# Optimization experiments

Hardware: AMD Instinct MI355X
Metric: run time of the kernel (lower is better)

## Reference

```python
import jax, jax.numpy as jnp
from jax import lax
import numpy as np

P = 7            # patch_size
NP = 10          # n_patches
WIN = 20         # window_size
STRIDE = 4       # window loop stride
EMB = 128        # embedding_dimension
L = WIN - P + 1  # valid-conv output side (14)
HALF = WIN // 2 - P // 2  # window start offset before clipping (7)


def _positions(H, W):
    # x outer, y inner, exactly matching the nested python loops in the source
    return np.array([(x, y) for x in range(0, H - WIN + 1, STRIDE)
                     for y in range(0, W - WIN + 1, STRIDE)], dtype=np.int32)


def _forward(images, Wp, bp, pos_emb, Wb, bb):
    B, C, H, W = images.shape
    BC = B * C
    pos = jnp.asarray(_positions(H, W))  # [Ppos, 2]

    def per_pos(p):
        x, y = p[0], p[1]
        xb0 = jnp.maximum(x - HALF, 0)          # clipped window start (x / cols)
        yb0 = jnp.maximum(y - HALF, 0)          # clipped window start (y / rows)
        winW = jnp.minimum(x - HALF + WIN, W) - xb0  # clipped window width
        winH = jnp.minimum(y - HALF + WIN, H) - yb0  # clipped window height
        # reference patch: rows y:y+P, cols x:x+P (from ORIGINAL data, as in source)
        ref = lax.dynamic_slice(images, (0, 0, y, x), (B, C, P, P)).reshape(BC, 1, P, P)
        # fixed-size window slice; upper bound never clips for our dims, lower-clip
        # handled by masking invalid candidate offsets below
        win = lax.dynamic_slice(images, (0, 0, yb0, xb0), (B, C, WIN, WIN)).reshape(BC, WIN, WIN)
        # grouped cross-correlation == torch conv2d(groups=BC) similarity
        sim = lax.conv_general_dilated(win[None], ref, (1, 1), 'VALID',
                                       feature_group_count=BC,
                                       dimension_numbers=('NCHW', 'OIHW', 'NCHW'))[0]  # [BC,L,L]
        valid = (jnp.arange(L)[:, None] <= winH - P) & (jnp.arange(L)[None, :] <= winW - P)
        sim = jnp.where(valid[None], sim, -jnp.inf)
        _, idx = lax.top_k(sim.reshape(BC, L * L), NP)  # [BC, NP]
        oy, ox = idx // L, idx % L  # row / col offsets inside the window

        def extract(w2, a, b):
            # source's meshgrid indexing yields the TRANSPOSED patch, flattened
            return lax.dynamic_slice(w2, (a, b), (P, P)).T.reshape(P * P)
        patches = jax.vmap(jax.vmap(extract, in_axes=(None, 0, 0)))(win, oy, ox)  # [BC,NP,P*P]
        # source bug kept: x_coords = row offset + x window start (and vice versa)
        return patches, oy + xb0, ox + yb0

    patches, xi, yi = jax.vmap(per_pos)(pos)  # [Ppos,BC,NP,49], [Ppos,BC,NP] int32 x2

    # NOTE: the TransformerEncoder output is discarded in the source; the actual
    # math is back_projection(projection(patches) + pos_emb).
    emb = patches.reshape(-1, B, C, NP, P * P) @ Wp + bp + pos_emb  # [Ppos,B,C,NP,EMB]
    den = (emb @ Wb + bb).reshape(-1, BC, NP, P, P)                 # [Ppos,BC,NP,P,P]

    img0 = images.reshape(BC, H, W)
    cnt0 = jnp.ones((BC, H, W), images.dtype)

    def upd(im, cn, x_i, y_i, d):
        reg = lax.dynamic_slice(im, (y_i, x_i), (P, P))
        c = lax.dynamic_slice(cn, (y_i, x_i), (P, P))
        im = lax.dynamic_update_slice(im, (reg * c + d) / (c + 1.0), (y_i, x_i))
        # source bug kept: counter incremented at transposed slice [x, y]
        ct = lax.dynamic_slice(cn, (x_i, y_i), (P, P)) + 1.0
        cn = lax.dynamic_update_slice(cn, ct, (x_i, y_i))
        return im, cn
    vupd = jax.vmap(upd)  # (b,c) planes are independent -> vectorize

    def n_step(carry, t):
        d, x_i, y_i = t
        return vupd(carry[0], carry[1], x_i, y_i, d), None

    def pos_step(carry, t):
        d, x_i, y_i = t  # d:[BC,NP,P,P]
        carry, _ = lax.scan(n_step, carry, (jnp.moveaxis(d, 1, 0), x_i.T, y_i.T))
        return carry, None

    (img, _), _ = lax.scan(pos_step, (img0, cnt0), (den, xi, yi))
    return img.reshape(B, C, H, W)


def setup_inputs() -> dict:
    key = jax.random.key(0)
    k0, k1, k2, k3 = jax.random.split(key, 4)
    B, C, H, W = 4, 8, 160, 160
    return {
        'images': jax.random.normal(k0, (B, C, H, W), jnp.float32),
        'Wp': jax.random.normal(k1, (P * P, EMB), jnp.float32) * 0.05,
        'bp': jnp.zeros((EMB,), jnp.float32),
        'pos_emb': jax.random.normal(k2, (1, NP, EMB), jnp.float32),
        'Wb': jax.random.normal(k3, (EMB, P * P), jnp.float32) * 0.05,
        'bb': jnp.zeros((P * P,), jnp.float32),
    }


def reference(images, Wp, bp, pos_emb, Wb, bb):
    return _forward(images, Wp, bp, pos_emb, Wb, bb)
```

## Files before the change

kernel.cpp:

```cpp
#include <hip/hip_runtime.h>

#define PS 7
#define NP 10
#define WIN 20
#define STR 4
#define LL 14
#define HALF 7
#define HH 160
#define WW 160
#define BCN 32
#define NX 36
#define PPOS 1296
#define EMBD 128
#define NTASK (BCN * PPOS * NP)
#define NEV (PPOS * NP)
#define CAP 512
#define NTILE 400

__global__ __launch_bounds__(256) void k_mk(const float* __restrict__ Wp,
                                            const float* __restrict__ bp,
                                            const float* __restrict__ pe,
                                            const float* __restrict__ Wb,
                                            const float* __restrict__ bb,
                                            float* __restrict__ M,
                                            float* __restrict__ K) {
    int t = blockIdx.x * 256 + threadIdx.x;
    if (t < 49 * 49) {
        int k = t / 49, d = t % 49;
        float acc = 0.f;
        for (int e = 0; e < EMBD; ++e) acc += Wp[k * EMBD + e] * Wb[e * 49 + d];
        M[t] = acc;
    } else if (t < 49 * 49 + NP * 49) {
        int u = t - 49 * 49;
        int n = u / 49, d = u % 49;
        float acc = bb[d];
        for (int e = 0; e < EMBD; ++e) acc += (bp[e] + pe[n * EMBD + e]) * Wb[e * 49 + d];
        K[u] = acc;
    }
}

__global__ __launch_bounds__(64) void k_sim(const float* __restrict__ img,
                                            unsigned* __restrict__ xy,
                                            float* __restrict__ pd) {
    int blk = blockIdx.x;
    int pos = blk % PPOS;
    int bc  = blk / PPOS;
    int lane = threadIdx.x;
    int ix = pos / NX, iy = pos % NX;
    int x = ix * STR, y = iy * STR;
    int xb0 = max(x - HALF, 0), yb0 = max(y - HALF, 0);
    int jmax = x + 6 - xb0;
    int imax = y + 6 - yb0;
    const float* plane = img + bc * (HH * WW);

    float v[4];
    int   qi[4];
#pragma unroll
    for (int s = 0; s < 4; ++s) {
        int q = lane + s * 64;
        qi[s] = q;
        float acc = -INFINITY;
        if (q < 196) {
            int i = q / 14, j = q % 14;
            const float* wbase = plane + (yb0 + i) * WW + (xb0 + j);
            float a2 = 0.f;
#pragma unroll
            for (int a = 0; a < PS; ++a)
#pragma unroll
                for (int b = 0; b < PS; ++b)
                    a2 += wbase[a * WW + b] * plane[(y + a) * WW + (x + b)];
            acc = (i > imax || j > jmax) ? -INFINITY : a2;
        }
        v[s] = acc;
    }

    int tbase = (bc * PPOS + pos) * NP;
    for (int n = 0; n < NP; ++n) {
        float bv = v[0]; int bi = qi[0];
#pragma unroll
        for (int s = 1; s < 4; ++s)
            if (v[s] > bv || (v[s] == bv && qi[s] < bi)) { bv = v[s]; bi = qi[s]; }
#pragma unroll
        for (int off = 32; off >= 1; off >>= 1) {
            float ov = __shfl_xor(bv, off);
            int   oi = __shfl_xor(bi, off);
            if (ov > bv || (ov == bv && oi < bi)) { bv = ov; bi = oi; }
        }
#pragma unroll
        for (int s = 0; s < 4; ++s)
            if (qi[s] == bi) v[s] = -INFINITY;

        int oy = bi / 14, ox = bi % 14;
        int x_i = oy + xb0;
        int y_i = ox + yb0;
        int row0 = yb0 + oy, col0 = xb0 + ox;
        int t = tbase + n;
        if (lane == 0) xy[t] = (unsigned)x_i | ((unsigned)y_i << 8);
        if (lane < 49) {
            int a = lane / 7, b = lane % 7;
            pd[(size_t)t * 49 + lane] = plane[(row0 + b) * WW + (col0 + a)];
        }
    }
}

__global__ __launch_bounds__(256) void k_den(float* __restrict__ pd,
                                             const float* __restrict__ Mg,
                                             const float* __restrict__ Kg) {
    __shared__ float Ps[256 * 49];
    int tid = threadIdx.x;
    size_t base = (size_t)blockIdx.x * (256 * 49);
    for (int i = tid; i < 256 * 49; i += 256) Ps[i] = pd[base + i];
    __syncthreads();

    int t = blockIdx.x * 256 + tid;
    int n = t % NP;
    float acc[49];
#pragma unroll
    for (int d = 0; d < 49; ++d) acc[d] = Kg[n * 49 + d];
    for (int k = 0; k < 49; ++k) {
        float p = Ps[tid * 49 + k];
        const float* mrow = Mg + k * 49;
#pragma unroll
        for (int d = 0; d < 49; ++d) acc[d] += p * mrow[d];
    }
    __syncthreads();
#pragma unroll
    for (int d = 0; d < 49; ++d) Ps[tid * 49 + d] = acc[d];
    __syncthreads();
    for (int i = tid; i < 256 * 49; i += 256) pd[base + i] = Ps[i];
}

__global__ __launch_bounds__(64) void k_build(const unsigned* __restrict__ xy,
                                              unsigned* __restrict__ lists,
                                              unsigned* __restrict__ counts) {
    int blk  = blockIdx.x;
    int bc   = blk / NTILE;
    int tile = blk % NTILE;
    int tx0 = (tile % 20) * 8, ty0 = (tile / 20) * 8;
    int tx1 = tx0 + 7, ty1 = ty0 + 7;
    int lane = threadIdx.x;
    const unsigned* xs = xy + bc * NEV;
    unsigned* lst = lists + (size_t)blk * CAP;

    int a0 = (tx0 <= 19) ? 0 : ((tx0 - 9) >> 2), a1 = min(35, (tx0 + 14) >> 2);
    int b0 = (ty0 <= 19) ? 0 : ((ty0 - 9) >> 2), b1 = min(35, (ty0 + 14) >> 2);
    if (a0 > b0) { int t0 = a0; a0 = b0; b0 = t0; int t1 = a1; a1 = b1; b1 = t1; }
    int lo0 = a0, lo1 = 0, len0, len1;
    if (b0 <= a1 + 1) { len0 = max(a1, b1) - lo0 + 1; len1 = 0; }
    else              { len0 = a1 - a0 + 1; lo1 = b0; len1 = b1 - b0 + 1; }
    int nU = len0 + len1;
    unsigned m = 65536u / (unsigned)nU + 1u;
    int npos = nU * nU;

    unsigned cnt = 0;
    for (int base = 0; base < npos; base += 64) {
        int k = base + lane;
        bool valid = k < npos;
        unsigned kk = valid ? (unsigned)k : 0u;
        int ki = (int)((kk * m) >> 16);
        int kj = (int)kk - ki * nU;
        int ix = (ki < len0) ? (lo0 + ki) : (lo1 + ki - len0);
        int iy = (kj < len0) ? (lo0 + kj) : (lo1 + kj - len0);
        int pos = ix * NX + iy;
        const unsigned* ep = xs + pos * NP;

        unsigned ev[NP];
#pragma unroll
        for (int n = 0; n < NP; ++n) ev[n] = ep[n];

        unsigned rel = 0;
        unsigned pk[NP];
#pragma unroll
        for (int n = 0; n < NP; ++n) {
            unsigned u = ev[n];
            int x_i = (int)(u & 255u);
            int y_i = (int)((u >> 8) & 255u);
            bool ih = (x_i <= tx1) && (x_i + 6 >= tx0) &&
                      (y_i <= ty1) && (y_i + 6 >= ty0);
            bool ch = (x_i <= ty1) && (x_i + 6 >= ty0) &&
                      (y_i <= tx1) && (y_i + 6 >= tx0);
            bool any = valid && (ih || ch);
            rel |= any ? (1u << n) : 0u;
            pk[n] = (unsigned)(pos * NP + n) | ((unsigned)x_i << 14) | ((unsigned)y_i << 22)
                  | (ih ? (1u << 30) : 0u) | (ch ? (1u << 31) : 0u);
        }
        int myc = __popc(rel);
        int scan = myc;
#pragma unroll
        for (int off = 1; off < 64; off <<= 1) {
            int o = __shfl_up(scan, off);
            scan += (lane >= off) ? o : 0;
        }
        int excl  = (int)cnt + scan - myc;
        int total = __shfl(scan, 63);
        int w = excl;
#pragma unroll
        for (int n = 0; n < NP; ++n) {
            if ((rel >> n) & 1u) { if (w < CAP) lst[w] = pk[n]; ++w; }
        }
        cnt += (unsigned)total;
    }
    if (cnt > CAP) cnt = CAP;
    unsigned cntp = (cnt + 7u) & ~7u;
    if (cntp > CAP) cntp = CAP;
    if (lane < (int)(cntp - cnt)) lst[cnt + lane] = 0u;
    if (lane == 0) counts[blk] = cntp;
}

__global__ __launch_bounds__(64) void k_apply(const float* __restrict__ img,
                                              const unsigned* __restrict__ lists,
                                              const unsigned* __restrict__ counts,
                                              const float* __restrict__ pd,
                                              float* __restrict__ out) {
    int blk  = blockIdx.x;
    int bc   = blk / NTILE;
    int tile = blk % NTILE;
    int tx0 = (tile % 20) * 8, ty0 = (tile / 20) * 8;
    int lane = threadIdx.x;
    int r  = ty0 + (lane >> 3);
    int cc = tx0 + (lane & 7);

    float im = img[bc * (HH * WW) + r * WW + cc];
    float c  = 1.0f;
    const unsigned* lst = lists + (size_t)blk * CAP;
    const float*    ds  = pd + (size_t)bc * ((size_t)NEV * 49);
    int cnt = (int)counts[blk];
    int vOff = (r * 7 + cc) * 4;

    for (int i = 0; i < cnt; i += 8) {
        unsigned eu[8];
        float    dv[8];
#pragma unroll
        for (int j = 0; j < 8; ++j)
            eu[j] = (unsigned)__builtin_amdgcn_readfirstlane((int)lst[i + j]);
#pragma unroll
        for (int j = 0; j < 8; ++j) {
            unsigned u = eu[j];
            int t    = (int)(u & 16383u);
            int x_i  = (int)((u >> 14) & 255u);
            int y_i  = (int)((u >> 22) & 255u);
            int sOff = (y_i * 7 + x_i) * 4;
            const char* dsb = (const char*)(ds + (size_t)t * 49);
            int boc = min(max(vOff - sOff, 0), 192);
            dv[j] = *(const float*)(dsb + boc);
        }
#pragma unroll
        for (int j = 0; j < 8; ++j) {
            unsigned u = eu[j];
            int x_i = (int)((u >> 14) & 255u);
            int y_i = (int)((u >> 22) & 255u);
            int dr = r - y_i, dc = cc - x_i;
            bool h = (u & (1u << 30)) && (((unsigned)dr <= 6u) & ((unsigned)dc <= 6u));
            float nim = fmaf(im, c, dv[j]) * __builtin_amdgcn_rcpf(c + 1.0f);
            im = h ? nim : im;
            int er = r - x_i, ec = cc - y_i;
            bool hc = (u >> 31) && (((unsigned)er <= 6u) & ((unsigned)ec <= 6u));
            c += hc ? 1.0f : 0.0f;
        }
    }
    out[bc * (HH * WW) + r * WW + cc] = im;
}

extern "C" void kernel_launch(void* const* d_in, const int* in_sizes, int n_in,
                              void* d_out, int out_size, void* d_ws, size_t ws_size,
                              hipStream_t stream) {
    const float* img = (const float*)d_in[0];
    const float* Wp  = (const float*)d_in[1];
    const float* bp  = (const float*)d_in[2];
    const float* pe  = (const float*)d_in[3];
    const float* Wb  = (const float*)d_in[4];
    const float* bb  = (const float*)d_in[5];
    float* out = (float*)d_out;

    float* wsf = (float*)d_ws;
    float*    M   = wsf;
    float*    K   = wsf + 2404;
    unsigned* xy  = (unsigned*)(wsf + 2896);
    float*    pd  = wsf + 2896 + NTASK;
    unsigned* lists  = (unsigned*)(pd + (size_t)NTASK * 49);
    unsigned* counts = lists + (size_t)BCN * NTILE * CAP;

    k_mk<<<12, 256, 0, stream>>>(Wp, bp, pe, Wb, bb, M, K);
    k_sim<<<BCN * PPOS, 64, 0, stream>>>(img, xy, pd);
    k_den<<<NTASK / 256, 256, 0, stream>>>(pd, M, K);
    k_build<<<BCN * NTILE, 64, 0, stream>>>(xy, lists, counts);
    k_apply<<<BCN * NTILE, 64, 0, stream>>>(img, lists, counts, pd, out);
}
```

Before: 353.6 us.

## Fuse list build into apply via LDS lists; simplify top-k argmax in sim

Measured after the change: 389.2 us. 1.1x slower.

```diff
diff --git a/kernel.cpp b/kernel.cpp
--- a/kernel.cpp
+++ b/kernel.cpp
@@ -52,16 +52,15 @@
     int jmax = x + 6 - xb0;
     int imax = y + 6 - yb0;
     const float* plane = img + bc * (HH * WW);
+    bool act = lane < 49;
 
     float v[4];
-    int   qi[4];
 #pragma unroll
     for (int s = 0; s < 4; ++s) {
-        int q = lane + s * 64;
-        qi[s] = q;
+        int q = 4 * lane + s;
+        int i = q / 14, j = q % 14;
         float acc = -INFINITY;
-        if (q < 196) {
-            int i = q / 14, j = q % 14;
+        if (act) {
             const float* wbase = plane + (yb0 + i) * WW + (xb0 + j);
             float a2 = 0.f;
 #pragma unroll
@@ -74,32 +73,36 @@
         v[s] = acc;
     }
 
+    int a_ = lane / 7, b_ = lane % 7;
+    int voffE = b_ * WW + a_;
     int tbase = (bc * PPOS + pos) * NP;
+
     for (int n = 0; n < NP; ++n) {
-        float bv = v[0]; int bi = qi[0];
+        float bv = v[0]; int bs = 0;
 #pragma unroll
         for (int s = 1; s < 4; ++s)
-            if (v[s] > bv || (v[s] == bv && qi[s] < bi)) { bv = v[s]; bi = qi[s]; }
+            if (v[s] > bv) { bv = v[s]; bs = s; }
+        float bvl = bv;
 #pragma unroll
         for (int off = 32; off >= 1; off >>= 1) {
             float ov = __shfl_xor(bv, off);
-            int   oi = __shfl_xor(bi, off);
-            if (ov > bv || (ov == bv && oi < bi)) { bv = ov; bi = oi; }
-        }
+            bv = fmaxf(bv, ov);
+        }
+        unsigned long long mk = __ballot(bvl == bv);
+        int w   = __ffsll(mk) - 1;
+        int bsw = __builtin_amdgcn_readlane(bs, w);
+        int bi  = 4 * w + bsw;
 #pragma unroll
         for (int s = 0; s < 4; ++s)
-            if (qi[s] == bi) v[s] = -INFINITY;
+            v[s] = (s == bsw && lane == w) ? -INFINITY : v[s];
 
         int oy = bi / 14, ox = bi % 14;
         int x_i = oy + xb0;
         int y_i = ox + yb0;
-        int row0 = yb0 + oy, col0 = xb0 + ox;
         int t = tbase + n;
         if (lane == 0) xy[t] = (unsigned)x_i | ((unsigned)y_i << 8);
-        if (lane < 49) {
-            int a = lane / 7, b = lane % 7;
-            pd[(size_t)t * 49 + lane] = plane[(row0 + b) * WW + (col0 + a)];
-        }
+        const float* src = plane + (yb0 + oy) * WW + (xb0 + ox);
+        if (act) pd[(size_t)t * 49 + lane] = src[voffE];
     }
 }
 
@@ -130,17 +133,21 @@
     for (int i = tid; i < 256 * 49; i += 256) pd[base + i] = Ps[i];
 }
 
-__global__ __launch_bounds__(64) void k_build(const unsigned* __restrict__ xy,
-                                              unsigned* __restrict__ lists,
-                                              unsigned* __restrict__ counts) {
-    int blk  = blockIdx.x;
-    int bc   = blk / NTILE;
-    int tile = blk % NTILE;
+__global__ __launch_bounds__(256) void k_apply(const float* __restrict__ img,
+                                               const unsigned* __restrict__ xy,
+                                               const float* __restrict__ pd,
+                                               float* __restrict__ out) {
+    __shared__ unsigned lsts[4][CAP];
+    int tid  = threadIdx.x;
+    int wv   = tid >> 6;
+    int lane = tid & 63;
+    int gt   = blockIdx.x * 4 + wv;
+    int bc   = gt / NTILE;
+    int tile = gt % NTILE;
     int tx0 = (tile % 20) * 8, ty0 = (tile / 20) * 8;
     int tx1 = tx0 + 7, ty1 = ty0 + 7;
-    int lane = threadIdx.x;
     const unsigned* xs = xy + bc * NEV;
-    unsigned* lst = lists + (size_t)blk * CAP;
+    unsigned* lst = lsts[wv];
 
     int a0 = (tx0 <= 19) ? 0 : ((tx0 - 9) >> 2), a1 = min(35, (tx0 + 14) >> 2);
     int b0 = (ty0 <= 19) ? 0 : ((ty0 - 9) >> 2), b1 = min(35, (ty0 + 14) >> 2);
@@ -159,9 +166,9 @@
         unsigned kk = valid ? (unsigned)k : 0u;
         int ki = (int)((kk * m) >> 16);
         int kj = (int)kk - ki * nU;
-        int ix = (ki < len0) ? (lo0 + ki) : (lo1 + ki - len0);
-        int iy = (kj < len0) ? (lo0 + kj) : (lo1 + kj - len0);
-        int pos = ix * NX + iy;
+        int ixp = (ki < len0) ? (lo0 + ki) : (lo1 + ki - len0);
+        int iyp = (kj < len0) ? (lo0 + kj) : (lo1 + kj - len0);
+        int pos = ixp * NX + iyp;
         const unsigned* ep = xs + pos * NP;
 
         unsigned ev[NP];
@@ -204,30 +211,16 @@
     unsigned cntp = (cnt + 7u) & ~7u;
     if (cntp > CAP) cntp = CAP;
     if (lane < (int)(cntp - cnt)) lst[cnt + lane] = 0u;
-    if (lane == 0) counts[blk] = cntp;
-}
-
-__global__ __launch_bounds__(64) void k_apply(const float* __restrict__ img,
-                                              const unsigned* __restrict__ lists,
-                                              const unsigned* __restrict__ counts,
-                                              const float* __restrict__ pd,
-                                              float* __restrict__ out) {
-    int blk  = blockIdx.x;
-    int bc   = blk / NTILE;
-    int tile = blk % NTILE;
-    int tx0 = (tile % 20) * 8, ty0 = (tile / 20) * 8;
-    int lane = threadIdx.x;
+    int cntN = (int)cntp;
+
     int r  = ty0 + (lane >> 3);
     int cc = tx0 + (lane & 7);
-
     float im = img[bc * (HH * WW) + r * WW + cc];
     float c  = 1.0f;
-    const unsigned* lst = lists + (size_t)blk * CAP;
-    const float*    ds  = pd + (size_t)bc * ((size_t)NEV * 49);
-    int cnt = (int)counts[blk];
+    const float* ds = pd + (size_t)bc * ((size_t)NEV * 49);
     int vOff = (r * 7 + cc) * 4;
 
-    for (int i = 0; i < cnt; i += 8) {
+    for (int i = 0; i < cntN; i += 8) {
         unsigned eu[8];
         float    dv[8];
 #pragma unroll
@@ -277,12 +270,9 @@
     float*    K   = wsf + 2404;
     unsigned* xy  = (unsigned*)(wsf + 2896);
     float*    pd  = wsf + 2896 + NTASK;
-    unsigned* lists  = (unsigned*)(pd + (size_t)NTASK * 49);
-    unsigned* counts = lists + (size_t)BCN * NTILE * CAP;
 
     k_mk<<<12, 256, 0, stream>>>(Wp, bp, pe, Wb, bb, M, K);
     k_sim<<<BCN * PPOS, 64, 0, stream>>>(img, xy, pd);
     k_den<<<NTASK / 256, 256, 0, stream>>>(pd, M, K);
-    k_build<<<BCN * NTILE, 64, 0, stream>>>(xy, lists, counts);
-    k_apply<<<BCN * NTILE, 64, 0, stream>>>(img, lists, counts, pd, out);
-}
+    k_apply<<<BCN * NTILE / 4, 256, 0, stream>>>(img, xy, pd, out);
+}
```
